# Performance work log

Hardware: AMD Instinct MI355X
Metric: run time of the kernel (lower is better)

## Reference

```python
import jax, jax.numpy as jnp
import numpy as np

EMBED_DIM = 1024
ATTN_DIM = 1024
BATCH = 4
SEQ = 2048


def setup_inputs() -> dict:
    key = jax.random.key(0)
    k1, k2, k3, k4 = jax.random.split(key, 4)
    embedded = jax.random.normal(k1, (BATCH, SEQ, EMBED_DIM), dtype=jnp.float32)
    # torch Linear weights have shape [out_features, in_features]
    scale = 1.0 / np.sqrt(EMBED_DIM)
    W_K = jax.random.uniform(k2, (ATTN_DIM, EMBED_DIM), dtype=jnp.float32, minval=-scale, maxval=scale)
    W_Q = jax.random.uniform(k3, (ATTN_DIM, EMBED_DIM), dtype=jnp.float32, minval=-scale, maxval=scale)
    W_V = jax.random.uniform(k4, (ATTN_DIM, EMBED_DIM), dtype=jnp.float32, minval=-scale, maxval=scale)
    return {"embedded": embedded, "W_K": W_K, "W_Q": W_Q, "W_V": W_V}


def reference(embedded, W_K, W_Q, W_V):
    # embedded: [B, L, E]; W_*: [A, E] (torch Linear layout, applied as x @ W.T)
    L = embedded.shape[1]
    A = W_K.shape[0]
    K = jnp.einsum('ble,ae->bla', embedded, W_K)
    Q = jnp.einsum('ble,ae->bla', embedded, W_Q)
    V = jnp.einsum('ble,ae->bla', embedded, W_V)
    att = jnp.einsum('bqa,bka->bqk', Q, K) / jnp.sqrt(jnp.float32(A))  # [B, L, L]
    causal = jnp.tril(jnp.ones((L, L), dtype=bool))  # lower-triangular mask
    att = jnp.where(causal, att, -jnp.inf)
    att = jax.nn.softmax(att, axis=-1)
    return jnp.einsum('bqk,bka->bqa', att, V)
```

## Files before the change

kernel.cpp:

```cpp
#include <hip/hip_runtime.h>
#include <hip/hip_bf16.h>
#include <stdint.h>

#define BATCH 4
#define SEQ   2048
#define EMB   1024
#define ADIM  1024

typedef __attribute__((ext_vector_type(8))) short  short8;
typedef __attribute__((ext_vector_type(4))) float  float4v;

static __device__ __forceinline__ unsigned short f2bf(float f) {
    unsigned int u = __float_as_uint(f);
    u += 0x7FFFu + ((u >> 16) & 1u);
    return (unsigned short)(u >> 16);
}

static __device__ __forceinline__ uint2 pack4(float4v v) {
    uint2 r;
    r.x = (unsigned)f2bf(v.x) | ((unsigned)f2bf(v.y) << 16);
    r.y = (unsigned)f2bf(v.z) | ((unsigned)f2bf(v.w) << 16);
    return r;
}

static __device__ __forceinline__ void gload16(const void* g, void* l) {
    __builtin_amdgcn_global_load_lds(
        (const __attribute__((address_space(1))) void*)g,
        (__attribute__((address_space(3))) void*)l, 16, 0, 0);
}

__global__ __launch_bounds__(256) void prep_kernel(
    const float* __restrict__ X,  const float* __restrict__ Wv,
    const float* __restrict__ Wq, const float* __restrict__ Wk,
    unsigned short* __restrict__ Xb, unsigned short* __restrict__ Wvb,
    unsigned short* __restrict__ WqT, unsigned short* __restrict__ WkT,
    float* __restrict__ rowsum)
{
    __shared__ unsigned short T[64][72];
    const int bI = blockIdx.x;
    if (bI < 4608) {
        const float* src; unsigned short* dst; int off;
        if (bI < 4096) { src = X;  dst = Xb;  off = bI; }
        else           { src = Wv; dst = Wvb; off = bI - 4096; }
        const int i = (off * 256 + threadIdx.x) * 8;
        float4v a = *(const float4v*)(src + i);
        float4v b = *(const float4v*)(src + i + 4);
        uint2 pa = pack4(a), pb = pack4(b);
        uint4 o; o.x = pa.x; o.y = pa.y; o.z = pb.x; o.w = pb.y;
        *(uint4*)(dst + i) = o;
        return;
    }
    if (bI < 4616) {
        const int i = ((bI - 4616) * 256 + threadIdx.x) * 4;
        *(float4v*)(rowsum + i) = float4v{0.f, 0.f, 0.f, 0.f};
        return;
    }
    const int z    = (bI - 4616) >> 8;
    const int tile = (bI - 4616) & 255;
    const int ti = tile >> 4;
    const int tj = tile & 15;
    const float* W = z ? Wk : Wq;
    unsigned short* WT = z ? WkT : WqT;
    const int t  = threadIdx.x;
    const int r  = t >> 2;
    const int c  = (t & 3) << 4;

    const float* src = W + (size_t)(ti * 64 + r) * EMB + tj * 64 + c;
    #pragma unroll
    for (int u = 0; u < 4; ++u) {
        float4v v = *(const float4v*)(src + 4 * u);
        uint2 p = pack4(v);
        *(uint2*)&T[r][c + 4 * u] = p;
    }
    __syncthreads();
    unsigned short tmp[16];
    #pragma unroll
    for (int u = 0; u < 16; ++u) tmp[u] = T[c + u][r];
    unsigned short* dst = WT + (size_t)(tj * 64 + r) * EMB + ti * 64 + c;
    *(uint4*)(dst)     = *(uint4*)&tmp[0];
    *(uint4*)(dst + 8) = *(uint4*)&tmp[8];
}

static __device__ __forceinline__ void gemm_core(
    const unsigned short* __restrict__ A, const unsigned short* __restrict__ B,
    int lda, int ldb, int m0, int n0, int kend,
    unsigned short* As, unsigned short* Bs, float4v acc[4][4])
{
    const int tid  = threadIdx.x;
    const int r    = tid >> 2;
    const int c8   = (tid & 3) << 3;
    const int lane = tid & 63;
    const int wave = tid >> 6;
    const int quad = lane >> 4;
    const int l16  = lane & 15;
    const int wm   = (wave >> 1) << 6;
    const int wn   = (wave & 1) << 6;

    const unsigned short* Ag = A + (size_t)(m0 + r) * lda + c8;
    const unsigned short* Bg = B + (size_t)(n0 + r) * ldb + c8;
    unsigned short* Al = As + tid * 8;
    unsigned short* Bl = Bs + tid * 8;
    const int niter = kend >> 5;

    #define ISSUE(k0, st) do { \
        unsigned short* al_ = Al + (st) * 4096; \
        unsigned short* bl_ = Bl + (st) * 4096; \
        gload16(Ag + (k0),                    al_); \
        gload16(Ag + (k0) + (size_t)64 * lda, al_ + 2048); \
        gload16(Bg + (k0),                    bl_); \
        gload16(Bg + (k0) + (size_t)64 * ldb, bl_ + 2048); \
    } while (0)

    ISSUE(0, 0);
    ISSUE(32, 1);

    int ci = 0, ii = 2;
    for (int it = 0; it < niter; ++it) {
        const int knext = (it + 2 < niter) ? ((it + 2) << 5) : 0;
        ISSUE(knext, ii);
        asm volatile("s_waitcnt vmcnt(8)" ::: "memory");
        asm volatile("s_barrier" ::: "memory");

        const unsigned short* Ah = As + ci * 4096;
        const unsigned short* Bh = Bs + ci * 4096;
        short8 af[4], bfr[4];
        #pragma unroll
        for (int i = 0; i < 4; ++i)
            af[i] = *(const short8*)&Ah[(wm + 16 * i + l16) * 32 + quad * 8];
        #pragma unroll
        for (int j = 0; j < 4; ++j)
            bfr[j] = *(const short8*)&Bh[(wn + 16 * j + l16) * 32 + quad * 8];
        #pragma unroll
        for (int i = 0; i < 4; ++i)
            #pragma unroll
            for (int j = 0; j < 4; ++j)
                acc[i][j] = __builtin_amdgcn_mfma_f32_16x16x32_bf16(af[i], bfr[j], acc[i][j], 0, 0, 0);

        asm volatile("s_barrier" ::: "memory");
        ci = (ci == 2) ? 0 : ci + 1;
        ii = (ii == 2) ? 0 : ii + 1;
    }
    asm volatile("s_waitcnt vmcnt(0)" ::: "memory");
    #undef ISSUE
}

#define DECL_TILE_IDX() \
    const int lane = threadIdx.x & 63; \
    const int wave = threadIdx.x >> 6; \
    const int quad = lane >> 4; \
    const int l16  = lane & 15; \
    const int wm   = (wave >> 1) << 6; \
    const int wn   = (wave & 1) << 6;

__global__ __launch_bounds__(256, 3) void m_kernel(
    const unsigned short* __restrict__ WkT, const unsigned short* __restrict__ WqT,
    unsigned short* __restrict__ Mt)
{
    __shared__ __align__(16) unsigned short As[3 * 128 * 32];
    __shared__ __align__(16) unsigned short Bs[3 * 128 * 32];
    const int m0 = (blockIdx.x >> 3) << 7;
    const int n0 = (blockIdx.x & 7) << 7;

    float4v acc[4][4];
    #pragma unroll
    for (int i = 0; i < 4; ++i)
        #pragma unroll
        for (int j = 0; j < 4; ++j)
            acc[i][j] = float4v{0.f, 0.f, 0.f, 0.f};

    gemm_core(WkT, WqT, EMB, EMB, m0, n0, EMB, As, Bs, acc);

    DECL_TILE_IDX();
    const float scale = 0.03125f;
    #pragma unroll
    for (int i = 0; i < 4; ++i)
        #pragma unroll
        for (int j = 0; j < 4; ++j)
            #pragma unroll
            for (int rr = 0; rr < 4; ++rr) {
                const int row = m0 + wm + 16 * i + quad * 4 + rr;
                const int col = n0 + wn + 16 * j + l16;
                Mt[(size_t)row * EMB + col] = f2bf(acc[i][j][rr] * scale);
            }
}

__global__ __launch_bounds__(256, 2) void qv_kernel(
    const unsigned short* __restrict__ Xb, const unsigned short* __restrict__ Mt,
    const unsigned short* __restrict__ Wvb,
    unsigned short* __restrict__ Qpb, unsigned short* __restrict__ Vtb)
{
    __shared__ __align__(16) unsigned short LDS[3 * 4096 + 3 * 8192];
    unsigned short* As = LDS;
    unsigned short* Bs = LDS + 3 * 4096;
    const int idx   = blockIdx.x;
    const int mlow  = idx & 7;
    const int n0    = ((idx >> 3) & 3) << 8;
    const int mhigh = (idx >> 5) & 7;
    const int z     = idx >> 8;
    const int m0    = ((mhigh << 3) | mlow) << 7;
    const unsigned short* B = (z == 0) ? Mt : Wvb;

    const int tid  = threadIdx.x;
    const int r    = tid >> 2;
    const int c8   = (tid & 3) << 3;
    const int lane = tid & 63;
    const int wave = tid >> 6;
    const int quad = lane >> 4;
    const int l16  = lane & 15;
    const int wm   = (wave >> 1) << 6;
    const int wn   = (wave & 1) << 7;

    float4v acc[4][8];
    #pragma unroll
    for (int i = 0; i < 4; ++i)
        #pragma unroll
        for (int j = 0; j < 8; ++j)
            acc[i][j] = float4v{0.f, 0.f, 0.f, 0.f};

    const unsigned short* Ag = Xb + (size_t)(m0 + r) * EMB + c8;
    const unsigned short* Bg = B  + (size_t)(n0 + r) * EMB + c8;
    unsigned short* Al = As + tid * 8;
    unsigned short* Bl = Bs + tid * 8;

    #define ISSUE_W(k0, st) do { \
        unsigned short* al_ = Al + (st) * 4096; \
        unsigned short* bl_ = Bl + (st) * 8192; \
        gload16(Ag + (k0),                     al_); \
        gload16(Ag + (k0) + (size_t)64  * EMB, al_ + 2048); \
        gload16(Bg + (k0),                     bl_); \
        gload16(Bg + (k0) + (size_t)64  * EMB, bl_ + 2048); \
        gload16(Bg + (k0) + (size_t)128 * EMB, bl_ + 4096); \
        gload16(Bg + (k0) + (size_t)192 * EMB, bl_ + 6144); \
    } while (0)

    ISSUE_W(0, 0);
    ISSUE_W(32, 1);

    int ci = 0, ii = 2;
    for (int it = 0; it < 32; ++it) {
        const int knext = (it + 2 < 32) ? ((it + 2) << 5) : 0;
        ISSUE_W(knext, ii);
        asm volatile("s_waitcnt vmcnt(12)" ::: "memory");
        asm volatile("s_barrier" ::: "memory");

        const unsigned short* Ah = As + ci * 4096;
        const unsigned short* Bh = Bs + ci * 8192;
        short8 af[4], bfr[8];
        #pragma unroll
        for (int i = 0; i < 4; ++i)
            af[i] = *(const short8*)&Ah[(wm + 16 * i + l16) * 32 + quad * 8];
        #pragma unroll
        for (int j = 0; j < 8; ++j)
            bfr[j] = *(const short8*)&Bh[(wn + 16 * j + l16) * 32 + quad * 8];
        #pragma unroll
        for (int i = 0; i < 4; ++i)
            #pragma unroll
            for (int j = 0; j < 8; ++j)
                acc[i][j] = __builtin_amdgcn_mfma_f32_16x16x32_bf16(af[i], bfr[j], acc[i][j], 0, 0, 0);

        asm volatile("s_barrier" ::: "memory");
        ci = (ci == 2) ? 0 : ci + 1;
        ii = (ii == 2) ? 0 : ii + 1;
    }
    asm volatile("s_waitcnt vmcnt(0)" ::: "memory");
    #undef ISSUE_W

    if (z == 0) {
        #pragma unroll
        for (int i = 0; i < 4; ++i)
            #pragma unroll
            for (int j = 0; j < 8; ++j)
                #pragma unroll
                for (int rr = 0; rr < 4; ++rr) {
                    const int row = m0 + wm + 16 * i + quad * 4 + rr;
                    const int col = n0 + wn + 16 * j + l16;
                    Qpb[(size_t)row * ADIM + col] = f2bf(acc[i][j][rr]);
                }
    } else {
        __syncthreads();
        unsigned short* T = LDS;
        #pragma unroll
        for (int i = 0; i < 4; ++i)
            #pragma unroll
            for (int j = 0; j < 8; ++j) {
                const int qrow = wm + 16 * i + quad * 4;
                const int acol = wn + 16 * j + l16;
                uint2 w;
                w.x = (unsigned)f2bf(acc[i][j][0]) | ((unsigned)f2bf(acc[i][j][1]) << 16);
                w.y = (unsigned)f2bf(acc[i][j][2]) | ((unsigned)f2bf(acc[i][j][3]) << 16);
                *(uint2*)&T[acol * 136 + qrow] = w;
            }
        __syncthreads();
        const int bb = m0 >> 11;
        const int l0 = m0 & (SEQ - 1);
        unsigned short* dst = Vtb + (((size_t)(bb * ADIM + n0 + tid)) << 11) + l0;
        #pragma unroll
        for (int u = 0; u < 16; ++u)
            *(uint4*)(dst + u * 8) = *(const uint4*)&T[tid * 136 + u * 8];
    }
}

__global__ __launch_bounds__(256, 3) void s_kernel(
    const unsigned short* __restrict__ Qpb, const unsigned short* __restrict__ Xb,
    unsigned short* __restrict__ E, float* __restrict__ rowsum)
{
    const int idx = blockIdx.x;
    const int b   = idx & 3;
    const int tri = idx >> 2;
    int qt = 0;
    while (((qt + 1) * (qt + 2)) / 2 <= tri) ++qt;
    const int kt = tri - (qt * (qt + 1)) / 2;
    const int q0 = qt << 7;
    const int k0 = kt << 7;

    __shared__ __align__(16) unsigned short As[3 * 128 * 32];
    __shared__ __align__(16) unsigned short Bs[3 * 128 * 32];

    float4v acc[4][4];
    #pragma unroll
    for (int i = 0; i < 4; ++i)
        #pragma unroll
        for (int j = 0; j < 4; ++j)
            acc[i][j] = float4v{0.f, 0.f, 0.f, 0.f};

    gemm_core(Qpb + (size_t)b * SEQ * ADIM, Xb + (size_t)b * SEQ * EMB,
              ADIM, EMB, q0, k0, EMB, As, Bs, acc);

    unsigned short* Eb = E + (size_t)b * SEQ * SEQ;
    float* rsb = rowsum + (size_t)b * SEQ;
    DECL_TILE_IDX();
    #pragma unroll
    for (int i = 0; i < 4; ++i)
        #pragma unroll
        for (int rr = 0; rr < 4; ++rr) {
            const int row = q0 + wm + 16 * i + quad * 4 + rr;
            float s = 0.f;
            #pragma unroll
            for (int j = 0; j < 4; ++j) {
                const int col = k0 + wn + 16 * j + l16;
                float e = (col <= row) ? __expf(acc[i][j][rr]) : 0.f;
                s += e;
                Eb[(size_t)row * SEQ + col] = f2bf(e);
            }
            s += __shfl_xor(s, 1);
            s += __shfl_xor(s, 2);
            s += __shfl_xor(s, 4);
            s += __shfl_xor(s, 8);
            if (l16 == 0) atomicAdd(&rsb[row], s);
        }
}

__global__ __launch_bounds__(256, 3) void pv_kernel(
    const unsigned short* __restrict__ E, const unsigned short* __restrict__ Vtb,
    const float* __restrict__ rowsum, float* __restrict__ out)
{
    const int idx = blockIdx.x;
    const int t   = (idx < 256) ? (15 - (idx >> 5)) : ((idx - 256) >> 5);
    const int rem = idx & 31;
    const int b   = rem >> 3;
    const int a0  = (rem & 7) << 7;
    const int q0  = t << 7;

    __shared__ __align__(16) unsigned short As[3 * 128 * 32];
    __shared__ __align__(16) unsigned short Bs[3 * 128 * 32];

    float4v acc[4][4];
    #pragma unroll
    for (int i = 0; i < 4; ++i)
        #pragma unroll
        for (int j = 0; j < 4; ++j)
            acc[i][j] = float4v{0.f, 0.f, 0.f, 0.f};

    gemm_core(E + (size_t)b * SEQ * SEQ, Vtb + (size_t)b * ADIM * SEQ,
              SEQ, SEQ, q0, a0, q0 + 128, As, Bs, acc);

    float* ob = out + (size_t)b * SEQ * ADIM;
    const float* rsb = rowsum + (size_t)b * SEQ;
    DECL_TILE_IDX();
    #pragma unroll
    for (int i = 0; i < 4; ++i)
        #pragma unroll
        for (int rr = 0; rr < 4; ++rr) {
            const int row = q0 + wm + 16 * i + quad * 4 + rr;
            const float inv = 1.0f / rsb[row];
            #pragma unroll
            for (int j = 0; j < 4; ++j) {
                const int col = a0 + wn + 16 * j + l16;
                ob[(size_t)row * ADIM + col] = acc[i][j][rr] * inv;
            }
        }
}

extern "C" void kernel_launch(void* const* d_in, const int* in_sizes, int n_in,
                              void* d_out, int out_size, void* d_ws, size_t ws_size,
                              hipStream_t stream)
{
    const float* X  = (const float*)d_in[0];
    const float* Wk = (const float*)d_in[1];
    const float* Wq = (const float*)d_in[2];
    const float* Wv = (const float*)d_in[3];
    float* out = (float*)d_out;

    const size_t MB = 1024 * 1024;
    char* ws = (char*)d_ws;
    unsigned short* Xb  = (unsigned short*)(ws);
    unsigned short* Wvb = (unsigned short*)(ws + 16 * MB);
    unsigned short* WqT = (unsigned short*)(ws + 18 * MB);
    unsigned short* WkT = (unsigned short*)(ws + 20 * MB);
    unsigned short* Mt  = (unsigned short*)(ws + 22 * MB);
    unsigned short* Qpb = (unsigned short*)(ws + 24 * MB);
    unsigned short* E   = (unsigned short*)(ws + 40 * MB);
    unsigned short* Vtb = (unsigned short*)(ws + 72 * MB);
    float*          rowsum = (float*)(ws + 88 * MB);

    hipLaunchKernelGGL(prep_kernel, dim3(5128), dim3(256), 0, stream,
                       X, Wv, Wq, Wk, Xb, Wvb, WqT, WkT, rowsum);
    hipLaunchKernelGGL(m_kernel, dim3(64), dim3(256), 0, stream, WkT, WqT, Mt);
    hipLaunchKernelGGL(qv_kernel, dim3(512), dim3(256), 0, stream,
                       Xb, Mt, Wvb, Qpb, Vtb);
    hipLaunchKernelGGL(s_kernel, dim3(4 * 136), dim3(256), 0, stream, Qpb, Xb, E, rowsum);
    hipLaunchKernelGGL(pv_kernel, dim3(512), dim3(256), 0, stream, E, Vtb, rowsum, out);
}
```

Before: 228.1 us.

## Fuse score and PV kernels with per-row-tile flags for dataflow overlap

Merges the masked-exp score kernel and the PV kernel into one launch. Score blocks publish completion through per-(batch, query-tile) atomic counters, and PV blocks spin on those counters before consuming E. This removes the kernel boundary so PV work on finished rows can overlap remaining score tiles. Score tiles are issued in reverse triangular order so the longest rows finish first. It relies on score blocks being scheduled before dependent PV blocks, and adds spin-wait and fence overhead. The prep kernel gains one block to zero the flag array, and the rowsum zeroing index bug is fixed.

```diff
diff --git a/kernel.cpp b/kernel.cpp
--- a/kernel.cpp
+++ b/kernel.cpp
@@ -50,13 +50,13 @@
         *(uint4*)(dst + i) = o;
         return;
     }
-    if (bI < 4616) {
-        const int i = ((bI - 4616) * 256 + threadIdx.x) * 4;
+    if (bI < 4617) {
+        const int i = ((bI - 4608) * 256 + threadIdx.x) * 4;
         *(float4v*)(rowsum + i) = float4v{0.f, 0.f, 0.f, 0.f};
         return;
     }
-    const int z    = (bI - 4616) >> 8;
-    const int tile = (bI - 4616) & 255;
+    const int z    = (bI - 4617) >> 8;
+    const int tile = (bI - 4617) & 255;
     const int ti = tile >> 4;
     const int tj = tile & 15;
     const float* W = z ? Wk : Wq;
@@ -189,7 +189,7 @@
     const unsigned short* __restrict__ Wvb,
     unsigned short* __restrict__ Qpb, unsigned short* __restrict__ Vtb)
 {
-    __shared__ __align__(16) unsigned short LDS[3 * 4096 + 3 * 8192];
+    __shared__ __align__(16) unsigned short LDS[36864];
     unsigned short* As = LDS;
     unsigned short* Bs = LDS + 3 * 4096;
     const int idx   = blockIdx.x;
@@ -300,95 +300,104 @@
     }
 }
 
-__global__ __launch_bounds__(256, 3) void s_kernel(
+__global__ __launch_bounds__(256, 3) void spv_kernel(
     const unsigned short* __restrict__ Qpb, const unsigned short* __restrict__ Xb,
-    unsigned short* __restrict__ E, float* __restrict__ rowsum)
-{
-    const int idx = blockIdx.x;
-    const int b   = idx & 3;
-    const int tri = idx >> 2;
-    int qt = 0;
-    while (((qt + 1) * (qt + 2)) / 2 <= tri) ++qt;
-    const int kt = tri - (qt * (qt + 1)) / 2;
-    const int q0 = qt << 7;
-    const int k0 = kt << 7;
-
+    unsigned short* __restrict__ E, float* __restrict__ rowsum,
+    unsigned* __restrict__ rowflag,
+    const unsigned short* __restrict__ Vtb, float* __restrict__ out)
+{
     __shared__ __align__(16) unsigned short As[3 * 128 * 32];
     __shared__ __align__(16) unsigned short Bs[3 * 128 * 32];
 
-    float4v acc[4][4];
-    #pragma unroll
-    for (int i = 0; i < 4; ++i)
-        #pragma unroll
-        for (int j = 0; j < 4; ++j)
-            acc[i][j] = float4v{0.f, 0.f, 0.f, 0.f};
-
-    gemm_core(Qpb + (size_t)b * SEQ * ADIM, Xb + (size_t)b * SEQ * EMB,
-              ADIM, EMB, q0, k0, EMB, As, Bs, acc);
-
-    unsigned short* Eb = E + (size_t)b * SEQ * SEQ;
-    float* rsb = rowsum + (size_t)b * SEQ;
-    DECL_TILE_IDX();
-    #pragma unroll
-    for (int i = 0; i < 4; ++i)
-        #pragma unroll
-        for (int rr = 0; rr < 4; ++rr) {
-            const int row = q0 + wm + 16 * i + quad * 4 + rr;
-            float s = 0.f;
-            #pragma unroll
-            for (int j = 0; j < 4; ++j) {
-                const int col = k0 + wn + 16 * j + l16;
-                float e = (col <= row) ? __expf(acc[i][j][rr]) : 0.f;
-                s += e;
-                Eb[(size_t)row * SEQ + col] = f2bf(e);
+    if (blockIdx.x < 544) {
+        const int idx = blockIdx.x;
+        const int b   = idx & 3;
+        const int tri = 135 - (idx >> 2);
+        int qt = 0;
+        while (((qt + 1) * (qt + 2)) / 2 <= tri) ++qt;
+        const int kt = tri - (qt * (qt + 1)) / 2;
+        const int q0 = qt << 7;
+        const int k0 = kt << 7;
+
+        float4v acc[4][4];
+        #pragma unroll
+        for (int i = 0; i < 4; ++i)
+            #pragma unroll
+            for (int j = 0; j < 4; ++j)
+                acc[i][j] = float4v{0.f, 0.f, 0.f, 0.f};
+
+        gemm_core(Qpb + (size_t)b * SEQ * ADIM, Xb + (size_t)b * SEQ * EMB,
+                  ADIM, EMB, q0, k0, EMB, As, Bs, acc);
+
+        unsigned short* Eb = E + (size_t)b * SEQ * SEQ;
+        float* rsb = rowsum + (size_t)b * SEQ;
+        DECL_TILE_IDX();
+        #pragma unroll
+        for (int i = 0; i < 4; ++i)
+            #pragma unroll
+            for (int rr = 0; rr < 4; ++rr) {
+                const int row = q0 + wm + 16 * i + quad * 4 + rr;
+                float s = 0.f;
+                #pragma unroll
+                for (int j = 0; j < 4; ++j) {
+                    const int col = k0 + wn + 16 * j + l16;
+                    float e = (col <= row) ? __expf(acc[i][j][rr]) : 0.f;
+                    s += e;
+                    Eb[(size_t)row * SEQ + col] = f2bf(e);
+                }
+                s += __shfl_xor(s, 1);
+                s += __shfl_xor(s, 2);
+                s += __shfl_xor(s, 4);
+                s += __shfl_xor(s, 8);
+                if (l16 == 0) atomicAdd(&rsb[row], s);
             }
-            s += __shfl_xor(s, 1);
-            s += __shfl_xor(s, 2);
-            s += __shfl_xor(s, 4);
-            s += __shfl_xor(s, 8);
-            if (l16 == 0) atomicAdd(&rsb[row], s);
+        __syncthreads();
+        if (threadIdx.x == 0) {
+            __threadfence();
+            __hip_atomic_fetch_add(&rowflag[b * 16 + qt], 1u,
+                                   __ATOMIC_RELEASE, __HIP_MEMORY_SCOPE_AGENT);
         }
-}
-
-__global__ __launch_bounds__(256, 3) void pv_kernel(
-    const unsigned short* __restrict__ E, const unsigned short* __restrict__ Vtb,
-    const float* __restrict__ rowsum, float* __restrict__ out)
-{
-    const int idx = blockIdx.x;
-    const int t   = (idx < 256) ? (15 - (idx >> 5)) : ((idx - 256) >> 5);
-    const int rem = idx & 31;
-    const int b   = rem >> 3;
-    const int a0  = (rem & 7) << 7;
-    const int q0  = t << 7;
-
-    __shared__ __align__(16) unsigned short As[3 * 128 * 32];
-    __shared__ __align__(16) unsigned short Bs[3 * 128 * 32];
-
-    float4v acc[4][4];
-    #pragma unroll
-    for (int i = 0; i < 4; ++i)
-        #pragma unroll
-        for (int j = 0; j < 4; ++j)
-            acc[i][j] = float4v{0.f, 0.f, 0.f, 0.f};
-
-    gemm_core(E + (size_t)b * SEQ * SEQ, Vtb + (size_t)b * ADIM * SEQ,
-              SEQ, SEQ, q0, a0, q0 + 128, As, Bs, acc);
-
-    float* ob = out + (size_t)b * SEQ * ADIM;
-    const float* rsb = rowsum + (size_t)b * SEQ;
-    DECL_TILE_IDX();
-    #pragma unroll
-    for (int i = 0; i < 4; ++i)
-        #pragma unroll
-        for (int rr = 0; rr < 4; ++rr) {
-            const int row = q0 + wm + 16 * i + quad * 4 + rr;
-            const float inv = 1.0f / rsb[row];
-            #pragma unroll
-            for (int j = 0; j < 4; ++j) {
-                const int col = a0 + wn + 16 * j + l16;
-                ob[(size_t)row * ADIM + col] = acc[i][j][rr] * inv;
+    } else {
+        const int p   = blockIdx.x - 544;
+        const int t   = (p < 256) ? (15 - (p >> 5)) : ((p - 256) >> 5);
+        const int rem = p & 31;
+        const int b   = rem >> 3;
+        const int a0  = (rem & 7) << 7;
+        const int q0  = t << 7;
+
+        if (threadIdx.x == 0) {
+            while (__hip_atomic_load(&rowflag[b * 16 + t], __ATOMIC_ACQUIRE,
+                                     __HIP_MEMORY_SCOPE_AGENT) < (unsigned)(t + 1))
+                __builtin_amdgcn_s_sleep(16);
+        }
+        __syncthreads();
+
+        float4v acc[4][4];
+        #pragma unroll
+        for (int i = 0; i < 4; ++i)
+            #pragma unroll
+            for (int j = 0; j < 4; ++j)
+                acc[i][j] = float4v{0.f, 0.f, 0.f, 0.f};
+
+        gemm_core(E + (size_t)b * SEQ * SEQ, Vtb + (size_t)b * ADIM * SEQ,
+                  SEQ, SEQ, q0, a0, q0 + 128, As, Bs, acc);
+
+        float* ob = out + (size_t)b * SEQ * ADIM;
+        const float* rsb = rowsum + (size_t)b * SEQ;
+        DECL_TILE_IDX();
+        #pragma unroll
+        for (int i = 0; i < 4; ++i)
+            #pragma unroll
+            for (int rr = 0; rr < 4; ++rr) {
+                const int row = q0 + wm + 16 * i + quad * 4 + rr;
+                const float inv = 1.0f / rsb[row];
+                #pragma unroll
+                for (int j = 0; j < 4; ++j) {
+                    const int col = a0 + wn + 16 * j + l16;
+                    ob[(size_t)row * ADIM + col] = acc[i][j][rr] * inv;
+                }
             }
-        }
+    }
 }
 
 extern "C" void kernel_launch(void* const* d_in, const int* in_sizes, int n_in,
@@ -411,13 +420,14 @@
     unsigned short* Qpb = (unsigned short*)(ws + 24 * MB);
     unsigned short* E   = (unsigned short*)(ws + 40 * MB);
     unsigned short* Vtb = (unsigned short*)(ws + 72 * MB);
-    float*          rowsum = (float*)(ws + 88 * MB);
-
-    hipLaunchKernelGGL(prep_kernel, dim3(5128), dim3(256), 0, stream,
+    float*          rowsum  = (float*)(ws + 88 * MB);
+    unsigned*       rowflag = (unsigned*)(ws + 88 * MB + 32768);
+
+    hipLaunchKernelGGL(prep_kernel, dim3(5129), dim3(256), 0, stream,
                        X, Wv, Wq, Wk, Xb, Wvb, WqT, WkT, rowsum);
     hipLaunchKernelGGL(m_kernel, dim3(64), dim3(256), 0, stream, WkT, WqT, Mt);
     hipLaunchKernelGGL(qv_kernel, dim3(512), dim3(256), 0, stream,
                        Xb, Mt, Wvb, Qpb, Vtb);
-    hipLaunchKernelGGL(s_kernel, dim3(4 * 136), dim3(256), 0, stream, Qpb, Xb, E, rowsum);
-    hipLaunchKernelGGL(pv_kernel, dim3(512), dim3(256), 0, stream, E, Vtb, rowsum, out);
-}
+    hipLaunchKernelGGL(spv_kernel, dim3(1056), dim3(256), 0, stream,
+                       Qpb, Xb, E, rowsum, rowflag, Vtb, out);
+}
```

Result: slower. 371.9 us (+63.1%).
